# Performance work log

Measured on AMD Instinct MI355X. Metric: run time of the kernel, lower is better.

The kernel has to match this reference:

```python
import jax, jax.numpy as jnp
import numpy as np

NUM_HEADS = 16
DIM_HEAD = 64
MAX_LEN = 512


def setup_inputs() -> dict:
    key = jax.random.key(0)
    ks = jax.random.split(key, 6)
    B, N, D = 16, 512, 1024
    inner = NUM_HEADS * DIM_HEAD  # 1024
    x = jax.random.normal(ks[0], (B, N, D), dtype=jnp.float32)
    w_qkv = jax.random.normal(ks[1], (D, 3 * inner), dtype=jnp.float32) * (D ** -0.5)
    b_qkv = jnp.zeros((3 * inner,), dtype=jnp.float32)
    rel_emb = jax.random.normal(ks[2], (2 * MAX_LEN - 1, NUM_HEADS), dtype=jnp.float32) * 0.02
    w_out = jax.random.normal(ks[3], (inner, D), dtype=jnp.float32) * (inner ** -0.5)
    b_out = jnp.zeros((D,), dtype=jnp.float32)
    return {"x": x, "w_qkv": w_qkv, "b_qkv": b_qkv, "rel_emb": rel_emb,
            "w_out": w_out, "b_out": b_out}


def reference(x, w_qkv, b_qkv, rel_emb, w_out, b_out):
    B, N, D = x.shape
    h, dh = NUM_HEADS, DIM_HEAD
    scale = dh ** -0.5
    qkv = x @ w_qkv + b_qkv  # (B, N, 3*h*dh)
    q, k, v = jnp.split(qkv, 3, axis=-1)
    def to_heads(t):
        return t.reshape(B, N, h, dh).transpose(0, 2, 1, 3)  # (B, h, N, dh)
    q, k, v = to_heads(q), to_heads(k), to_heads(v)
    dots = jnp.einsum('bhid,bhjd->bhij', q, k) * scale  # (B, h, N, N)
    # relative position bias: emb[(i - j) + max_len - 1] -> (N, N, h) -> (1, h, N, N)
    idx = jnp.arange(N)[:, None] - jnp.arange(N)[None, :] + (MAX_LEN - 1)
    bias = rel_emb[idx].transpose(2, 0, 1)[None]  # (1, h, N, N)
    attn = jax.nn.softmax(dots + bias, axis=-1)
    out = jnp.einsum('bhij,bhjd->bhid', attn, v)  # (B, h, N, dh)
    out = out.transpose(0, 2, 1, 3).reshape(B, N, h * dh)
    return out @ w_out + b_out
```

## Files before the change

### kernel.cpp

```cpp
#include <hip/hip_runtime.h>

#define SEQ    512
#define NH     16
#define DH     64
#define DMODEL 1024
#define NB     16
#define MROWS  (NB*SEQ)
#define MAXL   512

typedef _Float16 f16;
typedef f16  f16x8 __attribute__((ext_vector_type(8)));
typedef f16  f16x4 __attribute__((ext_vector_type(4)));
typedef float f32x4 __attribute__((ext_vector_type(4)));

__device__ static inline void gll16(const f16* g, f16* l) {
    __builtin_amdgcn_global_load_lds(
        (const __attribute__((address_space(1))) void*)(g),
        (__attribute__((address_space(3))) void*)(l), 16, 0, 0);
}

__global__ __launch_bounds__(256)
void cvt_f32_f16(const float* __restrict__ in, f16* __restrict__ out, int n)
{
    int i = (blockIdx.x * 256 + threadIdx.x) * 4;
    if (i < n) {
        float4 v = *(const float4*)(in + i);
        f16x4 h = { (f16)v.x, (f16)v.y, (f16)v.z, (f16)v.w };
        *(f16x4*)(out + i) = h;
    }
}

__global__ __launch_bounds__(256)
void transpose_cvt(const float* __restrict__ in, f16* __restrict__ out, int R, int C)
{
    __shared__ float tile[32][33];
    int c0 = blockIdx.x * 32, r0 = blockIdx.y * 32;
    int tx = threadIdx.x, ty = threadIdx.y;
    #pragma unroll
    for (int i = 0; i < 4; ++i)
        tile[ty + i * 8][tx] = in[(size_t)(r0 + ty + i * 8) * C + c0 + tx];
    __syncthreads();
    #pragma unroll
    for (int i = 0; i < 4; ++i)
        out[(size_t)(c0 + ty + i * 8) * R + r0 + tx] = (f16)tile[tx][ty + i * 8];
}

template<int MODE>
__global__ __launch_bounds__(256)
void gemm_mfma(const f16* __restrict__ A, const f16* __restrict__ Bt,
               const float* __restrict__ bias, int N, int K,
               float* __restrict__ Cout,
               f16* __restrict__ qb, f16* __restrict__ kb, f16* __restrict__ vb)
{
    __shared__ f16 As[128 * 32];
    __shared__ f16 Bs[128 * 32];
    const int t = threadIdx.x;
    const int lane = t & 63, w = t >> 6;
    const int quad = lane >> 4, l16 = lane & 15;
    const int m0 = blockIdx.y * 128, n0 = blockIdx.x * 128;
    const int wm = (w & 1) * 64, wn = (w >> 1) * 64;

    f32x4 acc[4][4];
    #pragma unroll
    for (int i = 0; i < 4; ++i)
        #pragma unroll
        for (int j = 0; j < 4; ++j)
            acc[i][j] = f32x4{0.f, 0.f, 0.f, 0.f};

    const int srow = t >> 2, scol = (t & 3) * 8;
    const f16* agp = A  + (size_t)(m0 + srow) * K + scol;
    const f16* bgp = Bt + (size_t)(n0 + srow) * K + scol;
    f16* alds = As + w * 512;
    f16* blds = Bs + w * 512;

    for (int k0 = 0; k0 < K; k0 += 32) {
        __syncthreads();
        gll16(agp + k0,          alds);
        gll16(agp + k0 + 64 * K, alds + 2048);
        gll16(bgp + k0,          blds);
        gll16(bgp + k0 + 64 * K, blds + 2048);
        __syncthreads();

        f16x8 af[4], bf[4];
        #pragma unroll
        for (int ms = 0; ms < 4; ++ms)
            af[ms] = *(const f16x8*)&As[(wm + ms * 16 + l16) * 32 + quad * 8];
        #pragma unroll
        for (int ns = 0; ns < 4; ++ns)
            bf[ns] = *(const f16x8*)&Bs[(wn + ns * 16 + l16) * 32 + quad * 8];
        #pragma unroll
        for (int ms = 0; ms < 4; ++ms)
            #pragma unroll
            for (int ns = 0; ns < 4; ++ns)
                acc[ms][ns] = __builtin_amdgcn_mfma_f32_16x16x32_f16(
                    af[ms], bf[ns], acc[ms][ns], 0, 0, 0);
    }

    if (MODE == 0) {
        #pragma unroll
        for (int ns = 0; ns < 4; ++ns) {
            int col = n0 + wn + ns * 16 + l16;
            float bv = bias[col];
            int which = col >> 10;
            int hh = (col & 1023) >> 6, d = col & 63;
            #pragma unroll
            for (int ms = 0; ms < 4; ++ms) {
                int rowb = m0 + wm + ms * 16 + quad * 4;
                int bb_ = rowb >> 9, n_ = rowb & 511;
                if (which == 2) {
                    f16x4 pk;
                    #pragma unroll
                    for (int reg = 0; reg < 4; ++reg)
                        pk[reg] = (f16)(acc[ms][ns][reg] + bv);
                    int c8s = ((n_ >> 3) & 7) ^ (d & 7);
                    f16* dst = vb + ((size_t)(bb_ * NH + hh) * DH + d) * SEQ
                                  + (n_ & ~63) + c8s * 8 + (n_ & 7);
                    *(f16x4*)dst = pk;
                } else if (which == 1) {
                    #pragma unroll
                    for (int reg = 0; reg < 4; ++reg) {
                        int n = n_ + reg;
                        int dd = (((d >> 3) ^ (n & 7)) * 8) + (d & 7);
                        kb[((size_t)(bb_ * NH + hh) * SEQ + n) * DH + dd] =
                            (f16)(acc[ms][ns][reg] + bv);
                    }
                } else {
                    #pragma unroll
                    for (int reg = 0; reg < 4; ++reg)
                        qb[((size_t)(bb_ * NH + hh) * SEQ + n_ + reg) * DH + d] =
                            (f16)(acc[ms][ns][reg] + bv);
                }
            }
        }
    } else {
        #pragma unroll
        for (int ns = 0; ns < 4; ++ns) {
            int col = n0 + wn + ns * 16 + l16;
            float bv = bias[col];
            #pragma unroll
            for (int ms = 0; ms < 4; ++ms) {
                int rowb = m0 + wm + ms * 16 + quad * 4;
                #pragma unroll
                for (int reg = 0; reg < 4; ++reg)
                    Cout[(size_t)(rowb + reg) * N + col] = acc[ms][ns][reg] + bv;
            }
        }
    }
}

__global__ __launch_bounds__(256)
void attn_mfma(const f16* __restrict__ qb, const f16* __restrict__ kb,
               const f16* __restrict__ vb, const float* __restrict__ rel,
               f16* __restrict__ ob)
{
    __shared__ f16 Ks[64 * 64];
    __shared__ f16 Vt[64 * 64];
    __shared__ f16 Pw[4][16 * 64];
    __shared__ float relh[1024];

    const int t = threadIdx.x;
    const int lane = t & 63, w = t >> 6;
    const int quad = lane >> 4, l16 = lane & 15;
    const int bid = blockIdx.x;
    const int bh = bid & 255, qt = bid >> 8;
    const int h = bh & 15, b = bh >> 4;

    for (int i = t; i < 2 * MAXL - 1; i += 256)
        relh[i] = rel[i * NH + h] * 1.44269504f;

    const f16* qrow = qb + ((size_t)bh * SEQ + qt * 64 + w * 16 + l16) * DH + quad * 8;
    f16x8 qf0 = *(const f16x8*)(qrow);
    f16x8 qf1 = *(const f16x8*)(qrow + 32);

    f32x4 o[4];
    #pragma unroll
    for (int dt = 0; dt < 4; ++dt) o[dt] = f32x4{0.f, 0.f, 0.f, 0.f};
    float lsum = 0.f;

    const f16* kpl = kb + (size_t)bh * SEQ * DH
                   + (size_t)(w * 16 + (lane >> 3)) * DH + (lane & 7) * 8;
    const f16* vpl = vb + (size_t)bh * DH * SEQ
                   + (size_t)(w * 16 + (lane >> 3)) * SEQ + (lane & 7) * 8;
    f16* kdst = Ks + w * 1024;
    f16* vdst = Vt + w * 1024;

    const int xr = l16 & 7;
    const int i0 = qt * 64 + w * 16 + l16;

    for (int kt = 0; kt < 8; ++kt) {
        __syncthreads();
        gll16(kpl + kt * 64 * DH,          kdst);
        gll16(kpl + kt * 64 * DH + 8 * DH, kdst + 512);
        gll16(vpl + kt * 64,               vdst);
        gll16(vpl + kt * 64 + 8 * SEQ,     vdst + 512);
        __syncthreads();

        f32x4 sT[4];
        #pragma unroll
        for (int mt = 0; mt < 4; ++mt) {
            const f16* kr = &Ks[(mt * 16 + l16) * 64];
            f16x8 a0 = *(const f16x8*)(kr + ((quad ^ xr) * 8));
            f16x8 a1 = *(const f16x8*)(kr + (((4 + quad) ^ xr) * 8));
            f32x4 c = f32x4{0.f, 0.f, 0.f, 0.f};
            c = __builtin_amdgcn_mfma_f32_16x16x32_f16(a0, qf0, c, 0, 0, 0);
            c = __builtin_amdgcn_mfma_f32_16x16x32_f16(a1, qf1, c, 0, 0, 0);
            sT[mt] = c;
        }

        const int cbase = i0 + (MAXL - 1) - kt * 64 - quad * 4;
        f16* pw = &Pw[w][0];
        #pragma unroll
        for (int mt = 0; mt < 4; ++mt) {
            f16x4 pk;
            #pragma unroll
            for (int reg = 0; reg < 4; ++reg) {
                float e = exp2f(fmaf(sT[mt][reg], 0.180336878f,
                                     relh[cbase - mt * 16 - reg]));
                lsum += e;
                pk[reg] = (f16)e;
            }
            int c8 = (mt * 2 + (quad >> 1)) ^ xr;
            *(f16x4*)&pw[l16 * 64 + c8 * 8 + (quad & 1) * 4] = pk;
        }
        __builtin_amdgcn_s_waitcnt(0xC07F);

        #pragma unroll
        for (int s2 = 0; s2 < 2; ++s2) {
            f16x8 pa = *(const f16x8*)&pw[l16 * 64 + (((s2 * 4 + quad) ^ xr) * 8)];
            #pragma unroll
            for (int dt = 0; dt < 4; ++dt) {
                const f16* vr = &Vt[(dt * 16 + l16) * 64];
                f16x8 vb8 = *(const f16x8*)(vr + (((s2 * 4 + quad) ^ xr) * 8));
                o[dt] = __builtin_amdgcn_mfma_f32_16x16x32_f16(pa, vb8, o[dt], 0, 0, 0);
            }
        }
    }

    lsum += __shfl_xor(lsum, 16, 64);
    lsum += __shfl_xor(lsum, 32, 64);
    #pragma unroll
    for (int reg = 0; reg < 4; ++reg) {
        float inv = 1.0f / __shfl(lsum, quad * 4 + reg, 64);
        size_t rbase = ((size_t)b * SEQ + qt * 64 + w * 16 + quad * 4 + reg) * DMODEL
                     + h * DH;
        #pragma unroll
        for (int dt = 0; dt < 4; ++dt)
            ob[rbase + dt * 16 + l16] = (f16)(o[dt][reg] * inv);
    }
}

extern "C" void kernel_launch(void* const* d_in, const int* in_sizes, int n_in,
                              void* d_out, int out_size, void* d_ws, size_t ws_size,
                              hipStream_t stream)
{
    const float* x    = (const float*)d_in[0];
    const float* wqkv = (const float*)d_in[1];
    const float* bqkv = (const float*)d_in[2];
    const float* rel  = (const float*)d_in[3];
    const float* wout = (const float*)d_in[4];
    const float* bout = (const float*)d_in[5];
    float* out = (float*)d_out;
    char* ws = (char*)d_ws;

    const size_t XH = (size_t)MROWS * DMODEL;
    f16* xh    = (f16*)(ws);
    f16* wqkvT = (f16*)(ws + 2 * XH);
    f16* woutT = wqkvT + (size_t)3 * DMODEL * DMODEL;
    f16* qbuf  = woutT + (size_t)DMODEL * DMODEL;
    f16* kbuf  = qbuf + XH;
    f16* vbuf  = kbuf + XH;
    f16* abuf  = vbuf + XH;

    cvt_f32_f16<<<XH / 1024, 256, 0, stream>>>(x, xh, (int)XH);
    transpose_cvt<<<dim3(3 * DMODEL / 32, DMODEL / 32), dim3(32, 8), 0, stream>>>(
        wqkv, wqkvT, DMODEL, 3 * DMODEL);
    transpose_cvt<<<dim3(DMODEL / 32, DMODEL / 32), dim3(32, 8), 0, stream>>>(
        wout, woutT, DMODEL, DMODEL);

    gemm_mfma<0><<<dim3(3 * DMODEL / 128, MROWS / 128), 256, 0, stream>>>(
        xh, wqkvT, bqkv, 3 * DMODEL, DMODEL, nullptr, qbuf, kbuf, vbuf);

    attn_mfma<<<dim3(NB * NH * (SEQ / 64)), 256, 0, stream>>>(
        qbuf, kbuf, vbuf, rel, abuf);

    gemm_mfma<1><<<dim3(DMODEL / 128, MROWS / 128), 256, 0, stream>>>(
        abuf, woutT, bout, DMODEL, DMODEL, out, nullptr, nullptr, nullptr);
}
```

Before: 251.8 us.

## Fuse prep kernels, double GEMM K-tile with swizzled LDS, store Q transposed

The three conversion/transpose launches are merged into one prep kernel to cut launch overhead. The GEMM K-tile grows from 32 to 64, with an XOR-swizzled LDS layout meant to avoid bank conflicts and halve the number of barrier pairs per output tile. Q is now written in a d-major transposed layout with vectorized f16x4 stores instead of scalar stores. In exchange, the attention kernel gathers Q with strided scalar loads, and LDS use per GEMM block doubles.

```diff
diff --git a/kernel.cpp b/kernel.cpp
--- a/kernel.cpp
+++ b/kernel.cpp
@@ -20,22 +20,30 @@
 }
 
 __global__ __launch_bounds__(256)
-void cvt_f32_f16(const float* __restrict__ in, f16* __restrict__ out, int n)
+void prep(const float* __restrict__ x, f16* __restrict__ xh,
+          const float* __restrict__ wqkv, f16* __restrict__ wqkvT,
+          const float* __restrict__ wout, f16* __restrict__ woutT)
 {
-    int i = (blockIdx.x * 256 + threadIdx.x) * 4;
-    if (i < n) {
-        float4 v = *(const float4*)(in + i);
+    const int bid = blockIdx.x, t = threadIdx.x;
+    if (bid < 8192) {
+        int i = (bid * 256 + t) * 4;
+        float4 v = *(const float4*)(x + i);
         f16x4 h = { (f16)v.x, (f16)v.y, (f16)v.z, (f16)v.w };
-        *(f16x4*)(out + i) = h;
-    }
-}
-
-__global__ __launch_bounds__(256)
-void transpose_cvt(const float* __restrict__ in, f16* __restrict__ out, int R, int C)
-{
+        *(f16x4*)(xh + i) = h;
+        return;
+    }
     __shared__ float tile[32][33];
-    int c0 = blockIdx.x * 32, r0 = blockIdx.y * 32;
-    int tx = threadIdx.x, ty = threadIdx.y;
+    const float* in; f16* out; int C, gx, gy;
+    if (bid < 8192 + 3072) {
+        int b2 = bid - 8192; in = wqkv; out = wqkvT; C = 3072;
+        gx = b2 % 96; gy = b2 / 96;
+    } else {
+        int b2 = bid - 11264; in = wout; out = woutT; C = 1024;
+        gx = b2 & 31; gy = b2 >> 5;
+    }
+    const int R = 1024;
+    int tx = t & 31, ty = t >> 5;
+    int c0 = gx * 32, r0 = gy * 32;
     #pragma unroll
     for (int i = 0; i < 4; ++i)
         tile[ty + i * 8][tx] = in[(size_t)(r0 + ty + i * 8) * C + c0 + tx];
@@ -52,11 +60,12 @@
                float* __restrict__ Cout,
                f16* __restrict__ qb, f16* __restrict__ kb, f16* __restrict__ vb)
 {
-    __shared__ f16 As[128 * 32];
-    __shared__ f16 Bs[128 * 32];
+    __shared__ f16 As[128 * 64];
+    __shared__ f16 Bs[128 * 64];
     const int t = threadIdx.x;
     const int lane = t & 63, w = t >> 6;
     const int quad = lane >> 4, l16 = lane & 15;
+    const int xr = l16 & 7;
     const int m0 = blockIdx.y * 128, n0 = blockIdx.x * 128;
     const int wm = (w & 1) * 64, wn = (w >> 1) * 64;
 
@@ -67,33 +76,39 @@
         for (int j = 0; j < 4; ++j)
             acc[i][j] = f32x4{0.f, 0.f, 0.f, 0.f};
 
-    const int srow = t >> 2, scol = (t & 3) * 8;
-    const f16* agp = A  + (size_t)(m0 + srow) * K + scol;
-    const f16* bgp = Bt + (size_t)(n0 + srow) * K + scol;
-    f16* alds = As + w * 512;
-    f16* blds = Bs + w * 512;
-
-    for (int k0 = 0; k0 < K; k0 += 32) {
+    const int sr8 = lane >> 3;
+    const int sc8 = (lane & 7) ^ sr8;
+    const f16* agp = A  + (size_t)(m0 + w * 32 + sr8) * K + sc8 * 8;
+    const f16* bgp = Bt + (size_t)(n0 + w * 32 + sr8) * K + sc8 * 8;
+    f16* asl = As + w * 2048;
+    f16* bsl = Bs + w * 2048;
+
+    for (int k0 = 0; k0 < K; k0 += 64) {
         __syncthreads();
-        gll16(agp + k0,          alds);
-        gll16(agp + k0 + 64 * K, alds + 2048);
-        gll16(bgp + k0,          blds);
-        gll16(bgp + k0 + 64 * K, blds + 2048);
+        #pragma unroll
+        for (int c = 0; c < 4; ++c) {
+            gll16(agp + k0 + c * 8 * K, asl + c * 512);
+            gll16(bgp + k0 + c * 8 * K, bsl + c * 512);
+        }
         __syncthreads();
-
-        f16x8 af[4], bf[4];
-        #pragma unroll
-        for (int ms = 0; ms < 4; ++ms)
-            af[ms] = *(const f16x8*)&As[(wm + ms * 16 + l16) * 32 + quad * 8];
-        #pragma unroll
-        for (int ns = 0; ns < 4; ++ns)
-            bf[ns] = *(const f16x8*)&Bs[(wn + ns * 16 + l16) * 32 + quad * 8];
-        #pragma unroll
-        for (int ms = 0; ms < 4; ++ms)
+        #pragma unroll
+        for (int ks = 0; ks < 2; ++ks) {
+            f16x8 af[4], bf[4];
+            #pragma unroll
+            for (int ms = 0; ms < 4; ++ms)
+                af[ms] = *(const f16x8*)&As[(wm + ms * 16 + l16) * 64
+                                            + (((ks * 4 + quad) ^ xr) * 8)];
             #pragma unroll
             for (int ns = 0; ns < 4; ++ns)
-                acc[ms][ns] = __builtin_amdgcn_mfma_f32_16x16x32_f16(
-                    af[ms], bf[ns], acc[ms][ns], 0, 0, 0);
+                bf[ns] = *(const f16x8*)&Bs[(wn + ns * 16 + l16) * 64
+                                            + (((ks * 4 + quad) ^ xr) * 8)];
+            #pragma unroll
+            for (int ms = 0; ms < 4; ++ms)
+                #pragma unroll
+                for (int ns = 0; ns < 4; ++ns)
+                    acc[ms][ns] = __builtin_amdgcn_mfma_f32_16x16x32_f16(
+                        af[ms], bf[ns], acc[ms][ns], 0, 0, 0);
+        }
     }
 
     if (MODE == 0) {
@@ -107,16 +122,21 @@
             for (int ms = 0; ms < 4; ++ms) {
                 int rowb = m0 + wm + ms * 16 + quad * 4;
                 int bb_ = rowb >> 9, n_ = rowb & 511;
-                if (which == 2) {
+                if (which == 0) {
+                    f16x4 pk;
+                    #pragma unroll
+                    for (int reg = 0; reg < 4; ++reg)
+                        pk[reg] = (f16)(acc[ms][ns][reg] + bv);
+                    *(f16x4*)(qb + ((size_t)(bb_ * NH + hh) * DH + d) * SEQ + n_) = pk;
+                } else if (which == 2) {
                     f16x4 pk;
                     #pragma unroll
                     for (int reg = 0; reg < 4; ++reg)
                         pk[reg] = (f16)(acc[ms][ns][reg] + bv);
                     int c8s = ((n_ >> 3) & 7) ^ (d & 7);
-                    f16* dst = vb + ((size_t)(bb_ * NH + hh) * DH + d) * SEQ
-                                  + (n_ & ~63) + c8s * 8 + (n_ & 7);
-                    *(f16x4*)dst = pk;
-                } else if (which == 1) {
+                    *(f16x4*)(vb + ((size_t)(bb_ * NH + hh) * DH + d) * SEQ
+                                 + (n_ & ~63) + c8s * 8 + (n_ & 7)) = pk;
+                } else {
                     #pragma unroll
                     for (int reg = 0; reg < 4; ++reg) {
                         int n = n_ + reg;
@@ -124,11 +144,6 @@
                         kb[((size_t)(bb_ * NH + hh) * SEQ + n) * DH + dd] =
                             (f16)(acc[ms][ns][reg] + bv);
                     }
-                } else {
-                    #pragma unroll
-                    for (int reg = 0; reg < 4; ++reg)
-                        qb[((size_t)(bb_ * NH + hh) * SEQ + n_ + reg) * DH + d] =
-                            (f16)(acc[ms][ns][reg] + bv);
                 }
             }
         }
@@ -168,9 +183,13 @@
     for (int i = t; i < 2 * MAXL - 1; i += 256)
         relh[i] = rel[i * NH + h] * 1.44269504f;
 
-    const f16* qrow = qb + ((size_t)bh * SEQ + qt * 64 + w * 16 + l16) * DH + quad * 8;
-    f16x8 qf0 = *(const f16x8*)(qrow);
-    f16x8 qf1 = *(const f16x8*)(qrow + 32);
+    const f16* qbase = qb + (size_t)bh * DH * SEQ + (qt * 64 + w * 16 + l16);
+    f16x8 qf0, qf1;
+    #pragma unroll
+    for (int j = 0; j < 8; ++j) {
+        qf0[j] = qbase[(quad * 8 + j) * SEQ];
+        qf1[j] = qbase[(quad * 8 + j + 32) * SEQ];
+    }
 
     f32x4 o[4];
     #pragma unroll
@@ -271,11 +290,7 @@
     f16* vbuf  = kbuf + XH;
     f16* abuf  = vbuf + XH;
 
-    cvt_f32_f16<<<XH / 1024, 256, 0, stream>>>(x, xh, (int)XH);
-    transpose_cvt<<<dim3(3 * DMODEL / 32, DMODEL / 32), dim3(32, 8), 0, stream>>>(
-        wqkv, wqkvT, DMODEL, 3 * DMODEL);
-    transpose_cvt<<<dim3(DMODEL / 32, DMODEL / 32), dim3(32, 8), 0, stream>>>(
-        wout, woutT, DMODEL, DMODEL);
+    prep<<<12288, 256, 0, stream>>>(x, xh, wqkv, wqkvT, wout, woutT);
 
     gemm_mfma<0><<<dim3(3 * DMODEL / 128, MROWS / 128), 256, 0, stream>>>(
         xh, wqkvT, bqkv, 3 * DMODEL, DMODEL, nullptr, qbuf, kbuf, vbuf);
```

New measurement: 239.5 us. 1.05x faster.
